# Kernel tuning notes

Hardware: AMD Instinct MI355X
Metric: run time of the kernel (lower is better)

Reference implementation:

```python
import jax, jax.numpy as jnp
import numpy as np

T, D, H, Z = 16384, 100, 50, 64
LN_EPS = 1e-6


def _ln(x, s, b):
    m = x.mean(-1, keepdims=True)
    v = ((x - m) ** 2).mean(-1, keepdims=True)
    return (x - m) / jnp.sqrt(v + LN_EPS) * s + b


def _gru_ln_scan(y, Wi, Wh, ls, lb):
    # Precompute all input projections once: [T, 3H]
    xi = y @ Wi
    h0 = jnp.zeros((Wh.shape[0],), y.dtype)

    def step(h, xi_t):
        hh = h @ Wh
        xr, xz, xn = jnp.split(xi_t, 3)
        hr, hz, hn = jnp.split(hh, 3)
        r = jax.nn.sigmoid(_ln(xr, ls[0], lb[0]) + _ln(hr, ls[1], lb[1]))
        z = jax.nn.sigmoid(_ln(xz, ls[2], lb[2]) + _ln(hz, ls[3], lb[3]))
        n = jnp.tanh(_ln(xn, ls[4], lb[4]) + r * _ln(hn, ls[5], lb[5]))
        h_new = (1.0 - z) * n + z * h
        return h_new, h_new

    _, hs = jax.lax.scan(step, h0, xi)
    return hs  # [T, H]


def setup_inputs() -> dict:
    key = jax.random.key(0)
    ks = jax.random.split(key, 6)
    sI = 1.0 / jnp.sqrt(jnp.float32(D))
    sH = 1.0 / jnp.sqrt(jnp.float32(H))
    sD = 1.0 / jnp.sqrt(jnp.float32(2 * H))
    return {
        "y": jax.random.normal(ks[0], (T, D), jnp.float32),
        "Wi_f": jax.random.normal(ks[1], (D, 3 * H), jnp.float32) * sI,
        "Wh_f": jax.random.normal(ks[2], (H, 3 * H), jnp.float32) * sH,
        "ln_s_f": jnp.ones((6, H), jnp.float32),
        "ln_b_f": jnp.zeros((6, H), jnp.float32),
        "Wi_b": jax.random.normal(ks[3], (D, 3 * H), jnp.float32) * sI,
        "Wh_b": jax.random.normal(ks[4], (H, 3 * H), jnp.float32) * sH,
        "ln_s_b": jnp.ones((6, H), jnp.float32),
        "ln_b_b": jnp.zeros((6, H), jnp.float32),
        "Wd": jax.random.normal(ks[5], (2 * H, 2 * Z), jnp.float32) * sD,
        "bd": jnp.zeros((2 * Z,), jnp.float32),
    }


def reference(y, Wi_f, Wh_f, ln_s_f, ln_b_f, Wi_b, Wh_b, ln_s_b, ln_b_b, Wd, bd):
    fwd = _gru_ln_scan(y, Wi_f, Wh_f, ln_s_f, ln_b_f)                       # [T, H]
    bwd = jnp.flip(_gru_ln_scan(jnp.flip(y, 0), Wi_b, Wh_b, ln_s_b, ln_b_b), 0)
    cc = jnp.concatenate([fwd, bwd], axis=-1)                               # [T, 2H]
    out = cc @ Wd + bd                                                      # [T, 2Z]
    z = Wd.shape[1] // 2
    mu, vflat = out[:, :z], out[:, z:]
    ev = jnp.exp(vflat)
    eye = jnp.eye(z, dtype=y.dtype)
    Sigma = eye * (ev + 1e-6)[:, None, :]   # diag(exp(v)+1e-6) per timestep
    J = eye * (1.0 / ev)[:, None, :]        # diag(1/exp(v)) per timestep
    h = mu / ev                             # J @ mu for diagonal J
    return Sigma, mu, J, h
```

## Files before the change

### kernel.cpp

```cpp
#include <hip/hip_runtime.h>

#define TT 16384
#define DD 100
#define HH 50
#define XG_STRIDE 160

#define CL 16
#define NCHUNK (TT / CL)
#define BURN 64

#define XROWS 16
#define NFILLB 512
#define OROWS 8

#define WS_XG 0
#define WS_HS (2 * TT * XG_STRIDE)

#define OFF_MU ((size_t)TT * 64 * 64)
#define OFF_J  (OFF_MU + (size_t)TT * 64)
#define OFF_H  (OFF_J + (size_t)TT * 64 * 64)

typedef float v2f __attribute__((ext_vector_type(2)));
typedef float v4f __attribute__((ext_vector_type(4)));

template <int CTRL>
__device__ __forceinline__ float dpp_add(float x) {
    const int y = __builtin_amdgcn_update_dpp(
        0, __builtin_bit_cast(int, x), CTRL, 0xf, 0xf, false);
    return x + __builtin_bit_cast(float, y);
}
__device__ __forceinline__ float wave_sum63(float x) {
    x = dpp_add<0x111>(x);
    x = dpp_add<0x112>(x);
    x = dpp_add<0x114>(x);
    x = dpp_add<0x118>(x);
    x = dpp_add<0x142>(x);
    x = dpp_add<0x143>(x);
    return x;
}
__device__ __forceinline__ float bcast_lane(float x, int l) {
    return __builtin_bit_cast(float,
        __builtin_amdgcn_readlane(__builtin_bit_cast(int, x), l));
}
__device__ __forceinline__ float fold_mean(float w, int L, int lane) {
    const float s = wave_sum63(w);
    const float cm = bcast_lane(s, 63) * 0.02f;
    return (lane == L) ? cm : w;
}

__global__ __launch_bounds__(192) void xprep_kernel(
    const float* __restrict__ y,
    const float* __restrict__ Wi_f, const float* __restrict__ Wi_b,
    const float* __restrict__ ls_f, const float* __restrict__ lb_f,
    const float* __restrict__ ls_b, const float* __restrict__ lb_b,
    float* __restrict__ xg, float* __restrict__ out)
{
    const int tid = threadIdx.x;
    const int dir = blockIdx.y;

    if (dir == 2) {
        const int fb = blockIdx.x;
        v4f* __restrict__ base = (fb < NFILLB)
            ? (v4f*)out : (v4f*)(out + OFF_J);
        const int sub = fb & (NFILLB - 1);
        const long QS = (long)TT * 1024;
        const v4f zz = {0.f, 0.f, 0.f, 0.f};
        const long stride = (long)NFILLB * 192;
        for (long q = (long)sub * 192 + tid; q < QS; q += stride)
            __builtin_nontemporal_store(zz, &base[q]);
        return;
    }

    const int t0  = blockIdx.x * XROWS;
    const float* __restrict__ Wi = dir ? Wi_b : Wi_f;
    const float* __restrict__ ls = dir ? ls_b : ls_f;
    const float* __restrict__ lb = dir ? lb_b : lb_f;

    __shared__ __align__(16) float yst[DD][XROWS];

    for (int idx = tid; idx < DD * XROWS; idx += 192) {
        const int r = idx / DD;
        const int k = idx - r * DD;
        const int row = dir ? (TT - 1 - (t0 + r)) : (t0 + r);
        yst[k][r] = y[(size_t)row * DD + k];
    }
    __syncthreads();

    const int g    = tid >> 6;
    const int lane = tid & 63;
    const bool act = lane < HH;
    const int col  = g * 50 + (act ? lane : 0);

    float acc[XROWS];
    #pragma unroll
    for (int r = 0; r < XROWS; ++r) acc[r] = 0.f;

    #pragma unroll 2
    for (int k = 0; k < DD; ++k) {
        const float w = Wi[k * 150 + col];
        const float4* yr = (const float4*)&yst[k][0];
        const float4 A = yr[0], B = yr[1], C = yr[2], D = yr[3];
        acc[0]  = fmaf(w, A.x, acc[0]);  acc[1]  = fmaf(w, A.y, acc[1]);
        acc[2]  = fmaf(w, A.z, acc[2]);  acc[3]  = fmaf(w, A.w, acc[3]);
        acc[4]  = fmaf(w, B.x, acc[4]);  acc[5]  = fmaf(w, B.y, acc[5]);
        acc[6]  = fmaf(w, B.z, acc[6]);  acc[7]  = fmaf(w, B.w, acc[7]);
        acc[8]  = fmaf(w, C.x, acc[8]);  acc[9]  = fmaf(w, C.y, acc[9]);
        acc[10] = fmaf(w, C.z, acc[10]); acc[11] = fmaf(w, C.w, acc[11]);
        acc[12] = fmaf(w, D.x, acc[12]); acc[13] = fmaf(w, D.y, acc[13]);
        acc[14] = fmaf(w, D.z, acc[14]); acc[15] = fmaf(w, D.w, acc[15]);
    }

    const int lrow = g * 100 + (act ? lane : 0);
    const float sc = ls[lrow], bi = lb[lrow];
    #pragma unroll
    for (int r = 0; r < XROWS; ++r) {
        const float a  = act ? acc[r] : 0.f;
        const float s  = bcast_lane(wave_sum63(a), 63);
        const float s2 = bcast_lane(wave_sum63(a * a), 63);
        const float mean = s * 0.02f;
        const float var  = s2 * 0.02f - mean * mean;
        const float rstd = rsqrtf(var + 1e-6f);
        if (act)
            xg[((size_t)dir * TT + (t0 + r)) * XG_STRIDE + col] =
                (acc[r] - mean) * rstd * sc + bi;
    }
}

__global__ __launch_bounds__(64, 1) void scan_kernel(
    const float* __restrict__ xg,
    const float* __restrict__ Wh_f, const float* __restrict__ Wh_b,
    const float* __restrict__ ls_f, const float* __restrict__ lb_f,
    const float* __restrict__ ls_b, const float* __restrict__ lb_b,
    float* __restrict__ hs)
{
    const int dir = blockIdx.y;
    const float* __restrict__ Wh = dir ? Wh_b : Wh_f;
    const float* __restrict__ ls = dir ? ls_b : ls_f;
    const float* __restrict__ lb = dir ? lb_b : lb_f;
    const float* __restrict__ xgd = xg + (size_t)dir * TT * XG_STRIDE;
    float* __restrict__ hsd = hs + (size_t)dir * TT * 64;

    const int lane = threadIdx.x;
    const bool act = lane < HH;

    const int cstart = blockIdx.x * CL;
    const int t0 = (cstart >= BURN) ? (cstart - BURN) : 0;
    const int tend = cstart + CL;

    __shared__ __align__(16) float hb[52];
    if (lane < 52) hb[lane] = 0.f;

    v2f wr2[26], wz2[26], wn2[26];
    #pragma unroll
    for (int p = 0; p < 26; ++p) {
        wr2[p] = (v2f){0.f, 0.f};
        wz2[p] = (v2f){0.f, 0.f};
        wn2[p] = (v2f){0.f, 0.f};
    }
    float s1 = 0.f, b1 = 0.f, s3 = 0.f, b3 = 0.f, s5 = 0.f, b5 = 0.f;
    if (act) {
        #pragma unroll
        for (int k = 0; k < HH; ++k) {
            const float a = Wh[k * 150 + lane];
            const float b = Wh[k * 150 + 50 + lane];
            const float c = Wh[k * 150 + 100 + lane];
            if (k & 1) { wr2[k >> 1].y = a; wz2[k >> 1].y = b; wn2[k >> 1].y = c; }
            else       { wr2[k >> 1].x = a; wz2[k >> 1].x = b; wn2[k >> 1].x = c; }
        }
        s1 = ls[50 + lane];  b1 = lb[50 + lane];
        s3 = ls[150 + lane]; b3 = lb[150 + lane];
        s5 = ls[250 + lane]; b5 = lb[250 + lane];
    }
    #pragma unroll
    for (int p = 0; p < 26; ++p) {
        wr2[p].x = fold_mean(wr2[p].x, 50, lane);
        wr2[p].y = fold_mean(wr2[p].y, 50, lane);
        wz2[p].x = fold_mean(wz2[p].x, 51, lane);
        wz2[p].y = fold_mean(wz2[p].y, 51, lane);
        wn2[p].x = fold_mean(wn2[p].x, 52, lane);
        wn2[p].y = fold_mean(wn2[p].y, 52, lane);
    }

    float hreg = 0.f;
    const int xl = act ? lane : 0;
    const float* __restrict__ x0 = xgd + (size_t)t0 * XG_STRIDE;
    float xr = x0[xl], xz = x0[50 + xl], xn = x0[100 + xl];
    float pxr = x0[XG_STRIDE + xl];
    float pxz = x0[XG_STRIDE + 50 + xl];
    float pxn = x0[XG_STRIDE + 100 + xl];

    #pragma unroll 1
    for (int t = t0; t < tend; ++t) {
        const int tp = (t + 2 < TT) ? (t + 2) : (TT - 1);
        const float* __restrict__ xp = xgd + (size_t)tp * XG_STRIDE;
        const float qxr = xp[xl], qxz = xp[50 + xl], qxn = xp[100 + xl];

        v2f ar0 = {0.f, 0.f}, ar1 = {0.f, 0.f};
        v2f az0 = {0.f, 0.f}, az1 = {0.f, 0.f};
        v2f an0 = {0.f, 0.f}, an1 = {0.f, 0.f};
        const float4* hb4 = reinterpret_cast<const float4*>(hb);
        #pragma unroll
        for (int q = 0; q < 13; ++q) {
            const float4 hv = hb4[q];
            const v2f h0 = {hv.x, hv.y};
            const v2f h1 = {hv.z, hv.w};
            ar0 = __builtin_elementwise_fma(h0, wr2[2 * q],     ar0);
            ar1 = __builtin_elementwise_fma(h1, wr2[2 * q + 1], ar1);
            az0 = __builtin_elementwise_fma(h0, wz2[2 * q],     az0);
            az1 = __builtin_elementwise_fma(h1, wz2[2 * q + 1], az1);
            an0 = __builtin_elementwise_fma(h0, wn2[2 * q],     an0);
            an1 = __builtin_elementwise_fma(h1, wn2[2 * q + 1], an1);
        }
        const float ar = (ar0.x + ar0.y) + (ar1.x + ar1.y);
        const float az = (az0.x + az0.y) + (az1.x + az1.y);
        const float an = (an0.x + an0.y) + (an1.x + an1.y);

        const float mr = bcast_lane(ar, 50);
        const float mz = bcast_lane(az, 51);
        const float mn = bcast_lane(an, 52);

        const float qrv = act ? ar * ar : 0.f;
        const float qzv = act ? az * az : 0.f;
        const float qnv = act ? an * an : 0.f;
        const float Sr = bcast_lane(wave_sum63(qrv), 63);
        const float Sz = bcast_lane(wave_sum63(qzv), 63);
        const float Sn = bcast_lane(wave_sum63(qnv), 63);

        const float i50 = 0.02f;
        const float vr = fmaf(-mr, mr, Sr * i50);
        const float vz = fmaf(-mz, mz, Sz * i50);
        const float vn = fmaf(-mn, mn, Sn * i50);
        const float rr = rsqrtf(vr + 1e-6f);
        const float rz = rsqrtf(vz + 1e-6f);
        const float rn = rsqrtf(vn + 1e-6f);
        const float hrl = (ar - mr) * rr * s1 + b1;
        const float hzl = (az - mz) * rz * s3 + b3;
        const float hnl = (an - mn) * rn * s5 + b5;

        const float r = __builtin_amdgcn_rcpf(1.f + __expf(-(xr + hrl)));
        const float z = __builtin_amdgcn_rcpf(1.f + __expf(-(xz + hzl)));
        const float e2 = __expf(2.f * (xn + r * hnl));
        const float n = 1.f - 2.f * __builtin_amdgcn_rcpf(e2 + 1.f);
        const float hnew = fmaf(z, hreg - n, n);

        if (act) {
            hb[lane] = hnew;
            if (t >= cstart) hsd[(size_t)t * 64 + lane] = hnew;
        }
        hreg = act ? hnew : 0.f;

        xr = pxr; xz = pxz; xn = pxn;
        pxr = qxr; pxz = qxz; pxn = qxn;
    }
}

__global__ __launch_bounds__(128) void outdiag_kernel(
    const float* __restrict__ hs, const float* __restrict__ Wd,
    const float* __restrict__ bd, float* __restrict__ out)
{
    const int t0 = blockIdx.x * OROWS;
    const int j  = threadIdx.x;

    __shared__ __align__(16) float ccs[DD][OROWS];
    __shared__ float os[OROWS][128];

    for (int idx = j; idx < DD * OROWS; idx += 128) {
        const int k = idx >> 3;
        const int r = idx & 7;
        const int t = t0 + r;
        ccs[k][r] = (k < 50)
            ? hs[(size_t)t * 64 + k]
            : hs[(size_t)(TT + (TT - 1 - t)) * 64 + (k - 50)];
    }
    __syncthreads();

    float acc[OROWS];
    const float b = bd[j];
    #pragma unroll
    for (int r = 0; r < OROWS; ++r) acc[r] = b;

    #pragma unroll 2
    for (int k = 0; k < DD; ++k) {
        const float w = Wd[k * 128 + j];
        const float4* cr = (const float4*)&ccs[k][0];
        const float4 A = cr[0], B4 = cr[1];
        acc[0] = fmaf(w, A.x,  acc[0]); acc[1] = fmaf(w, A.y,  acc[1]);
        acc[2] = fmaf(w, A.z,  acc[2]); acc[3] = fmaf(w, A.w,  acc[3]);
        acc[4] = fmaf(w, B4.x, acc[4]); acc[5] = fmaf(w, B4.y, acc[5]);
        acc[6] = fmaf(w, B4.z, acc[6]); acc[7] = fmaf(w, B4.w, acc[7]);
    }
    #pragma unroll
    for (int r = 0; r < OROWS; ++r) os[r][j] = acc[r];
    __syncthreads();

    if (j < 64) {
        const int d = j & 3;
        #pragma unroll
        for (int r = 0; r < OROWS; ++r) {
            const int t = t0 + r;
            const float mu  = os[r][j];
            const float evv = __expf(os[r][64 + j]);
            out[OFF_MU + (size_t)t * 64 + j] = mu;
            out[OFF_H  + (size_t)t * 64 + j] = mu / evv;
            const float se = evv + 1e-6f;
            float4 s4;
            s4.x = (d == 0) ? se : 0.f;  s4.y = (d == 1) ? se : 0.f;
            s4.z = (d == 2) ? se : 0.f;  s4.w = (d == 3) ? se : 0.f;
            ((float4*)out)[(size_t)t * 1024 + j * 16 + (j >> 2)] = s4;
        }
    } else {
        const int i = j - 64;
        const int d = i & 3;
        float4* __restrict__ jo4 = (float4*)(out + OFF_J);
        #pragma unroll
        for (int r = 0; r < OROWS; ++r) {
            const int t = t0 + r;
            const float evv = __expf(os[r][j]);
            const float je = 1.f / evv;
            float4 j4;
            j4.x = (d == 0) ? je : 0.f;  j4.y = (d == 1) ? je : 0.f;
            j4.z = (d == 2) ? je : 0.f;  j4.w = (d == 3) ? je : 0.f;
            jo4[(size_t)t * 1024 + i * 16 + (i >> 2)] = j4;
        }
    }
}

extern "C" void kernel_launch(void* const* d_in, const int* in_sizes, int n_in,
                              void* d_out, int out_size, void* d_ws, size_t ws_size,
                              hipStream_t stream)
{
    const float* y    = (const float*)d_in[0];
    const float* Wi_f = (const float*)d_in[1];
    const float* Wh_f = (const float*)d_in[2];
    const float* ls_f = (const float*)d_in[3];
    const float* lb_f = (const float*)d_in[4];
    const float* Wi_b = (const float*)d_in[5];
    const float* Wh_b = (const float*)d_in[6];
    const float* ls_b = (const float*)d_in[7];
    const float* lb_b = (const float*)d_in[8];
    const float* Wd   = (const float*)d_in[9];
    const float* bd   = (const float*)d_in[10];

    float* out = (float*)d_out;
    float* ws  = (float*)d_ws;
    float* xg  = ws + WS_XG;
    float* hsb = ws + WS_HS;

    xprep_kernel<<<dim3(TT / XROWS, 3), dim3(192), 0, stream>>>(
        y, Wi_f, Wi_b, ls_f, lb_f, ls_b, lb_b, xg, out);
    scan_kernel<<<dim3(NCHUNK, 2), dim3(64), 0, stream>>>(
        xg, Wh_f, Wh_b, ls_f, lb_f, ls_b, lb_b, hsb);
    outdiag_kernel<<<dim3(TT / OROWS), dim3(128), 0, stream>>>(
        hsb, Wd, bd, out);
}
```

Measured before the change: 259.6 us.

## Fuse bidirectional GRU scan with output head into one kernel

Merges the scan kernel and the output/diagonal kernel. Each block now runs one wave per direction over the same 16-step chunk of output rows, with the backward wave mapped to the mirrored chunk. Hidden states go into shared memory, and after a barrier both waves compute the dense head and write Sigma, mu, J and h. This drops the hs round trip through global memory and one kernel launch. In exchange the block count halves (1024 blocks of 128 threads instead of 2048 of 64), and the head work now sits behind the serial scan in every block.

```diff
diff --git a/kernel.cpp b/kernel.cpp
--- a/kernel.cpp
+++ b/kernel.cpp
@@ -11,10 +11,8 @@
 
 #define XROWS 16
 #define NFILLB 512
-#define OROWS 8
 
 #define WS_XG 0
-#define WS_HS (2 * TT * XG_STRIDE)
 
 #define OFF_MU ((size_t)TT * 64 * 64)
 #define OFF_J  (OFF_MU + (size_t)TT * 64)
@@ -126,29 +124,36 @@
     }
 }
 
-__global__ __launch_bounds__(64, 1) void scan_kernel(
+__global__ __launch_bounds__(128, 1) void scanhead_kernel(
     const float* __restrict__ xg,
     const float* __restrict__ Wh_f, const float* __restrict__ Wh_b,
     const float* __restrict__ ls_f, const float* __restrict__ lb_f,
     const float* __restrict__ ls_b, const float* __restrict__ lb_b,
-    float* __restrict__ hs)
+    const float* __restrict__ Wd, const float* __restrict__ bd,
+    float* __restrict__ out)
 {
-    const int dir = blockIdx.y;
+    const int tid  = threadIdx.x;
+    const int wid  = tid >> 6;
+    const int lane = tid & 63;
+    const int dir  = wid;
+    const int blk  = blockIdx.x;
+
     const float* __restrict__ Wh = dir ? Wh_b : Wh_f;
     const float* __restrict__ ls = dir ? ls_b : ls_f;
     const float* __restrict__ lb = dir ? lb_b : lb_f;
     const float* __restrict__ xgd = xg + (size_t)dir * TT * XG_STRIDE;
-    float* __restrict__ hsd = hs + (size_t)dir * TT * 64;
-
-    const int lane = threadIdx.x;
+
     const bool act = lane < HH;
 
-    const int cstart = blockIdx.x * CL;
+    const int cstart = dir ? (TT - (blk + 1) * CL) : (blk * CL);
+    const int rbase  = blk * CL;
     const int t0 = (cstart >= BURN) ? (cstart - BURN) : 0;
     const int tend = cstart + CL;
 
-    __shared__ __align__(16) float hb[52];
-    if (lane < 52) hb[lane] = 0.f;
+    __shared__ __align__(16) float ccs[DD][CL];
+    __shared__ __align__(16) float os[CL][128];
+    __shared__ __align__(16) float hb[2][52];
+    if (lane < 52) hb[wid][lane] = 0.f;
 
     v2f wr2[26], wz2[26], wn2[26];
     #pragma unroll
@@ -198,7 +203,7 @@
         v2f ar0 = {0.f, 0.f}, ar1 = {0.f, 0.f};
         v2f az0 = {0.f, 0.f}, az1 = {0.f, 0.f};
         v2f an0 = {0.f, 0.f}, an1 = {0.f, 0.f};
-        const float4* hb4 = reinterpret_cast<const float4*>(hb);
+        const float4* hb4 = reinterpret_cast<const float4*>(&hb[wid][0]);
         #pragma unroll
         for (int q = 0; q < 13; ++q) {
             const float4 hv = hb4[q];
@@ -244,60 +249,49 @@
         const float hnew = fmaf(z, hreg - n, n);
 
         if (act) {
-            hb[lane] = hnew;
-            if (t >= cstart) hsd[(size_t)t * 64 + lane] = hnew;
+            hb[wid][lane] = hnew;
+            if (t >= cstart) {
+                const int rr2 = dir ? (TT - 1 - t - rbase) : (t - rbase);
+                ccs[dir * 50 + lane][rr2] = hnew;
+            }
         }
         hreg = act ? hnew : 0.f;
 
         xr = pxr; xz = pxz; xn = pxn;
         pxr = qxr; pxz = qxz; pxn = qxn;
     }
-}
-
-__global__ __launch_bounds__(128) void outdiag_kernel(
-    const float* __restrict__ hs, const float* __restrict__ Wd,
-    const float* __restrict__ bd, float* __restrict__ out)
-{
-    const int t0 = blockIdx.x * OROWS;
-    const int j  = threadIdx.x;
-
-    __shared__ __align__(16) float ccs[DD][OROWS];
-    __shared__ float os[OROWS][128];
-
-    for (int idx = j; idx < DD * OROWS; idx += 128) {
-        const int k = idx >> 3;
-        const int r = idx & 7;
-        const int t = t0 + r;
-        ccs[k][r] = (k < 50)
-            ? hs[(size_t)t * 64 + k]
-            : hs[(size_t)(TT + (TT - 1 - t)) * 64 + (k - 50)];
-    }
+
     __syncthreads();
 
-    float acc[OROWS];
-    const float b = bd[j];
-    #pragma unroll
-    for (int r = 0; r < OROWS; ++r) acc[r] = b;
+    const int j = tid;
+    float acc[CL];
+    const float bj = bd[j];
+    #pragma unroll
+    for (int r = 0; r < CL; ++r) acc[r] = bj;
 
     #pragma unroll 2
     for (int k = 0; k < DD; ++k) {
         const float w = Wd[k * 128 + j];
         const float4* cr = (const float4*)&ccs[k][0];
-        const float4 A = cr[0], B4 = cr[1];
-        acc[0] = fmaf(w, A.x,  acc[0]); acc[1] = fmaf(w, A.y,  acc[1]);
-        acc[2] = fmaf(w, A.z,  acc[2]); acc[3] = fmaf(w, A.w,  acc[3]);
-        acc[4] = fmaf(w, B4.x, acc[4]); acc[5] = fmaf(w, B4.y, acc[5]);
-        acc[6] = fmaf(w, B4.z, acc[6]); acc[7] = fmaf(w, B4.w, acc[7]);
-    }
-    #pragma unroll
-    for (int r = 0; r < OROWS; ++r) os[r][j] = acc[r];
+        const float4 A = cr[0], B4 = cr[1], C4 = cr[2], D4 = cr[3];
+        acc[0]  = fmaf(w, A.x,  acc[0]);  acc[1]  = fmaf(w, A.y,  acc[1]);
+        acc[2]  = fmaf(w, A.z,  acc[2]);  acc[3]  = fmaf(w, A.w,  acc[3]);
+        acc[4]  = fmaf(w, B4.x, acc[4]);  acc[5]  = fmaf(w, B4.y, acc[5]);
+        acc[6]  = fmaf(w, B4.z, acc[6]);  acc[7]  = fmaf(w, B4.w, acc[7]);
+        acc[8]  = fmaf(w, C4.x, acc[8]);  acc[9]  = fmaf(w, C4.y, acc[9]);
+        acc[10] = fmaf(w, C4.z, acc[10]); acc[11] = fmaf(w, C4.w, acc[11]);
+        acc[12] = fmaf(w, D4.x, acc[12]); acc[13] = fmaf(w, D4.y, acc[13]);
+        acc[14] = fmaf(w, D4.z, acc[14]); acc[15] = fmaf(w, D4.w, acc[15]);
+    }
+    #pragma unroll
+    for (int r = 0; r < CL; ++r) os[r][j] = acc[r];
     __syncthreads();
 
     if (j < 64) {
         const int d = j & 3;
         #pragma unroll
-        for (int r = 0; r < OROWS; ++r) {
-            const int t = t0 + r;
+        for (int r = 0; r < CL; ++r) {
+            const int t = rbase + r;
             const float mu  = os[r][j];
             const float evv = __expf(os[r][64 + j]);
             out[OFF_MU + (size_t)t * 64 + j] = mu;
@@ -313,8 +307,8 @@
         const int d = i & 3;
         float4* __restrict__ jo4 = (float4*)(out + OFF_J);
         #pragma unroll
-        for (int r = 0; r < OROWS; ++r) {
-            const int t = t0 + r;
+        for (int r = 0; r < CL; ++r) {
+            const int t = rbase + r;
             const float evv = __expf(os[r][j]);
             const float je = 1.f / evv;
             float4 j4;
@@ -344,12 +338,9 @@
     float* out = (float*)d_out;
     float* ws  = (float*)d_ws;
     float* xg  = ws + WS_XG;
-    float* hsb = ws + WS_HS;
 
     xprep_kernel<<<dim3(TT / XROWS, 3), dim3(192), 0, stream>>>(
         y, Wi_f, Wi_b, ls_f, lb_f, ls_b, lb_b, xg, out);
-    scan_kernel<<<dim3(NCHUNK, 2), dim3(64), 0, stream>>>(
-        xg, Wh_f, Wh_b, ls_f, lb_f, ls_b, lb_b, hsb);
-    outdiag_kernel<<<dim3(TT / OROWS), dim3(128), 0, stream>>>(
-        hsb, Wd, bd, out);
-}
+    scanhead_kernel<<<dim3(NCHUNK), dim3(128), 0, stream>>>(
+        xg, Wh_f, Wh_b, ls_f, lb_f, ls_b, lb_b, Wd, bd, out);
+}
```

After: 248.1 us. -4.4%, faster.
